# Performance work log

Hardware: AMD Instinct MI355X
Metric: run time of the kernel (lower is better)

## Reference

```python
import jax, jax.numpy as jnp
import numpy as np

N = 10000      # nodes
E = 100000     # edges
D = 768        # hidden = heads * head_dim
H = 4          # heads
C = D // H     # 192 per-head channels
EDIM = 16      # edge feature dim
NREL = 10      # num relations
L = 3          # num TransformerConv layers


def setup_inputs() -> dict:
    key = jax.random.key(0)
    ks = jax.random.split(key, 16)
    s = 0.02
    x = jax.random.normal(ks[0], (N, D), jnp.float32)
    edge_index = jax.random.randint(ks[1], (2, E), 0, N, jnp.int32)
    rel = jax.random.randint(ks[2], (E,), 0, NREL).astype(jnp.float32)
    w = jax.random.uniform(ks[3], (E,), jnp.float32)
    edge_attr = jnp.stack([rel, w], axis=1)  # [E, 2]: (relation_id, weight)
    rel_emb = jax.random.normal(ks[4], (NREL, EDIM - 1), jnp.float32) * s
    W_edge = jax.random.normal(ks[5], (EDIM, EDIM), jnp.float32) * s
    b_edge = jnp.zeros((EDIM,), jnp.float32)
    Wk = jax.random.normal(ks[6], (L, D, D), jnp.float32) * s
    bk = jnp.zeros((L, D), jnp.float32)
    Wq = jax.random.normal(ks[7], (L, D, D), jnp.float32) * s
    bq = jnp.zeros((L, D), jnp.float32)
    Wv = jax.random.normal(ks[8], (L, D, D), jnp.float32) * s
    bv = jnp.zeros((L, D), jnp.float32)
    We = jax.random.normal(ks[9], (L, EDIM, D), jnp.float32) * s   # lin_edge, no bias (PyG)
    Wskip = jax.random.normal(ks[10], (L, D, D), jnp.float32) * s  # root/skip linear
    bskip = jnp.zeros((L, D), jnp.float32)
    ln_g = jnp.ones((D,), jnp.float32)
    ln_b = jnp.zeros((D,), jnp.float32)
    return dict(x=x, edge_attr=edge_attr, edge_index=edge_index, rel_emb=rel_emb,
                W_edge=W_edge, b_edge=b_edge, Wk=Wk, bk=bk, Wq=Wq, bq=bq,
                Wv=Wv, bv=bv, We=We, Wskip=Wskip, bskip=bskip, ln_g=ln_g, ln_b=ln_b)


def reference(x, edge_attr, edge_index, rel_emb, W_edge, b_edge,
              Wk, bk, Wq, bq, Wv, bv, We, Wskip, bskip, ln_g, ln_b):
    src, dst = edge_index[0], edge_index[1]
    # _process_edge_features: embed relation id, concat weight, project
    rel_ids = jnp.clip(jax.lax.stop_gradient(edge_attr[:, 0]).astype(jnp.int32), 0, NREL - 1)
    ef = jnp.concatenate([rel_emb[rel_ids], edge_attr[:, 1:2]], axis=-1) @ W_edge + b_edge  # [E,16]
    scale = 1.0 / np.sqrt(C)
    h = x  # input_proj is Identity (input_dim == hidden_dim)
    for l in range(L):
        q = (h @ Wq[l] + bq[l]).reshape(N, H, C)
        k = (h @ Wk[l] + bk[l]).reshape(N, H, C)
        v = (h @ Wv[l] + bv[l]).reshape(N, H, C)
        e = (ef @ We[l]).reshape(E, H, C)           # per-edge embedding
        kj = k[src] + e                              # [E,H,C]
        alpha = jnp.einsum('ehc,ehc->eh', q[dst], kj) * scale  # [E,H]
        # scatter-softmax over incoming edges of each destination node
        m = jax.ops.segment_max(jax.lax.stop_gradient(alpha), dst, num_segments=N)
        a = jnp.exp(alpha - m[dst])
        denom = jax.ops.segment_sum(a, dst, num_segments=N)
        a = a / (denom[dst] + 1e-16)
        msg = (v[src] + e) * a[..., None]            # [E,H,C]
        out = jax.ops.segment_sum(msg.reshape(E, H * C), dst, num_segments=N)
        h = out + h @ Wskip[l] + bskip[l]            # root_weight skip connection
        if l < L - 1:
            h = jax.nn.gelu(h, approximate=False)    # dropout: eval mode -> identity
    mu = jnp.mean(h, axis=-1, keepdims=True)
    var = jnp.mean((h - mu) ** 2, axis=-1, keepdims=True)
    h = (h - mu) / jnp.sqrt(var + 1e-5) * ln_g + ln_b
    return jnp.mean(h, axis=0)  # global_mean_pool over single graph -> [D]
```

## Files before the change

### kernel.cpp

```cpp
#include <hip/hip_runtime.h>
#include <hip/hip_bf16.h>
#include <math.h>
#include <stdint.h>

#define NN 10000
#define EE 100000
#define DD 768
#define HH 4
#define CC 192
#define EDIM 16
#define NREL 10
#define MP 10112
#define NQ2 3200
#define SCALE 0.07216878364870322f

using short8  = __attribute__((ext_vector_type(8))) short;
using floatx4 = __attribute__((ext_vector_type(4))) float;


__device__ __forceinline__ float b2f(short u) {
    union { unsigned int i; float f; } t;
    t.i = ((unsigned int)(unsigned short)u) << 16;
    return t.f;
}

__device__ __forceinline__ short f2b(float f) {
    __hip_bfloat16 h = __float2bfloat16(f);
    short r;
    __builtin_memcpy(&r, &h, 2);
    return r;
}

__device__ __forceinline__ __hip_bfloat16 rd_any(const void* p, long long j, int bf) {
    if (bf) return ((const __hip_bfloat16*)p)[j];
    return __float2bfloat16(((const float*)p)[j]);
}

__device__ __forceinline__ void gload16(const __hip_bfloat16* g, __hip_bfloat16* l) {
    __builtin_amdgcn_global_load_lds(
        (const __attribute__((address_space(1))) unsigned int*)g,
        (__attribute__((address_space(3))) unsigned int*)l, 16, 0, 0);
}

__global__ __launch_bounds__(256) void detect_zero(const void* edge_attr,
                                                   int* flag, int* counts) {
    int i = blockIdx.x * 256 + threadIdx.x;
    if (i < NN) counts[i] = 0;
    if (blockIdx.x == 0 && threadIdx.x < 64) {
        const unsigned short* p = (const unsigned short*)edge_attr;
        int nz = (p[4 * threadIdx.x] != 0) ? 1 : 0;
        unsigned long long m = __ballot(nz);
        if (threadIdx.x == 0) *flag = (__popcll(m) > 8) ? 1 : 0;
    }
}


__global__ __launch_bounds__(256) void cvt_big(
    const void* x, const void* We, const int* flag,
    __hip_bfloat16* hb, __hip_bfloat16* Web) {
    long long i = (long long)blockIdx.x * 256 + threadIdx.x;
    int bf = *flag;
    const long long NX = (long long)NN * DD;
    const long long NE2 = 3LL * EDIM * DD;
    if (i < NX) { hb[i] = rd_any(x, i, bf); return; } i -= NX;
    if (i < NE2) { Web[i] = rd_any(We, i, bf); return; } i -= NE2;
    if (i < (long long)(MP - NN) * DD) hb[(long long)NN * DD + i] = __float2bfloat16(0.0f);
}

__global__ __launch_bounds__(256) void cvt_small(
    const void* ea, const void* rel, const void* Wed, const void* bed,
    const void* bk, const void* bq, const void* bv, const void* bs,
    const void* lg, const void* lb, const int* flag,
    __hip_bfloat16* eab, __hip_bfloat16* relb, __hip_bfloat16* Wedb,
    __hip_bfloat16* bedb, __hip_bfloat16* ballb, __hip_bfloat16* lgb,
    __hip_bfloat16* lbb) {
    long long i = (long long)blockIdx.x * 256 + threadIdx.x;
    int bf = *flag;
    if (i < 2LL * EE) { eab[i] = rd_any(ea, i, bf); return; } i -= 2LL * EE;
    if (i < NREL * (EDIM - 1)) { relb[i] = rd_any(rel, i, bf); return; } i -= NREL * (EDIM - 1);
    if (i < EDIM * EDIM) { Wedb[i] = rd_any(Wed, i, bf); return; } i -= EDIM * EDIM;
    if (i < EDIM) { bedb[i] = rd_any(bed, i, bf); return; } i -= EDIM;
    if (i < 3 * NQ2) {
        int l = (int)(i / NQ2), c = (int)(i % NQ2);
        const void* src; long long off;
        if (c < 768)       { src = bq; off = (long long)l * DD + c; }
        else if (c < 1536) { src = bk; off = (long long)l * DD + (c - 768); }
        else if (c < 2304) { src = bv; off = (long long)l * DD + (c - 1536); }
        else if (c < 3072) { src = bs; off = (long long)l * DD + (c - 2304); }
        else { ballb[i] = __float2bfloat16(0.0f); return; }
        ballb[i] = rd_any(src, off, bf); return;
    } i -= 3 * NQ2;
    if (i < DD) { lgb[i] = rd_any(lg, i, bf); return; } i -= DD;
    if (i < DD) { lbb[i] = rd_any(lb, i, bf); return; }
}

__global__ __launch_bounds__(256) void wt_all(
    const void* Wq, const void* Wk, const void* Wv, const void* Ws,
    const int* flag, __hip_bfloat16* Wt3) {
    __shared__ __hip_bfloat16 tile[32][33];
    int mm = blockIdx.y;
    int l = mm >> 2, m = mm & 3;
    const void* src = (m == 0) ? Wq : (m == 1) ? Wk : (m == 2) ? Wv : Ws;
    int bx = blockIdx.x;
    int tr = bx / 24, tc = bx % 24;
    int k0 = tr * 32, c0 = tc * 32;
    int t = threadIdx.x;
    int rr = t >> 5, cc = t & 31;
    int bf = *flag;
    long long base = (long long)l * DD * DD;
#pragma unroll
    for (int p = 0; p < 4; p++)
        tile[p * 8 + rr][cc] =
            rd_any(src, base + (long long)(k0 + p * 8 + rr) * DD + c0 + cc, bf);
    __syncthreads();
    __hip_bfloat16* dst = Wt3 + (size_t)l * NQ2 * DD + (size_t)(m * 768 + c0) * DD + k0;
#pragma unroll
    for (int p = 0; p < 4; p++)
        dst[(size_t)(p * 8 + rr) * DD + cc] = tile[cc][p * 8 + rr];
}

__global__ __launch_bounds__(256) void mq_kernel(
    const void* Wq, const void* bq, const int* flag,
    const __hip_bfloat16* __restrict__ Web, __hip_bfloat16* __restrict__ Wt3,
    __hip_bfloat16* __restrict__ ballb) {
    __shared__ float WeS[16][193];
    const int lh = blockIdx.y, l = lh >> 2, hh = lh & 3;
    const int t = threadIdx.x;
    const int bf = *flag;
    for (int i = t; i < 16 * 192; i += 256) {
        int j = i / 192, c = i % 192;
        WeS[j][c] = (float)Web[(size_t)l * EDIM * DD + (size_t)j * DD + hh * CC + c];
    }
    __syncthreads();
    const int k = blockIdx.x * 64 + (t >> 2);
    const int j0 = (t & 3) * 4;
    float s0 = 0.f, s1 = 0.f, s2 = 0.f, s3 = 0.f;
    if (bf) {
        const short8* qp = (const short8*)((const __hip_bfloat16*)Wq +
            ((size_t)l * DD + k) * DD + hh * CC);
#pragma unroll 4
        for (int ch = 0; ch < 24; ch++) {
            short8 v = qp[ch];
#pragma unroll
            for (int u = 0; u < 8; u++) {
                float w = b2f(v[u]);
                int c = ch * 8 + u;
                s0 += w * WeS[j0 + 0][c]; s1 += w * WeS[j0 + 1][c];
                s2 += w * WeS[j0 + 2][c]; s3 += w * WeS[j0 + 3][c];
            }
        }
    } else {
        const float4* qp = (const float4*)((const float*)Wq +
            ((size_t)l * DD + k) * DD + hh * CC);
#pragma unroll 4
        for (int ch = 0; ch < 48; ch++) {
            float4 v = qp[ch];
            float wv[4] = {v.x, v.y, v.z, v.w};
#pragma unroll
            for (int u = 0; u < 4; u++) {
                float w = wv[u];
                int c = ch * 4 + u;
                s0 += w * WeS[j0 + 0][c]; s1 += w * WeS[j0 + 1][c];
                s2 += w * WeS[j0 + 2][c]; s3 += w * WeS[j0 + 3][c];
            }
        }
    }
    const size_t base = (size_t)l * NQ2 * DD;
    const int row = 3072 + hh * 16 + j0;
    Wt3[base + (size_t)(row + 0) * DD + k] = __float2bfloat16(s0);
    Wt3[base + (size_t)(row + 1) * DD + k] = __float2bfloat16(s1);
    Wt3[base + (size_t)(row + 2) * DD + k] = __float2bfloat16(s2);
    Wt3[base + (size_t)(row + 3) * DD + k] = __float2bfloat16(s3);
    const int prow = 3136 + hh * 16 + j0;
#pragma unroll
    for (int i = 0; i < 4; i++)
        Wt3[base + (size_t)(prow + i) * DD + k] = __float2bfloat16(0.0f);
    if (blockIdx.x == 0 && t < 4) {
        float b0 = 0.f, b1 = 0.f, b2 = 0.f, b3 = 0.f;
        for (int c = 0; c < CC; c++) {
            float w = (float)rd_any(bq, (long long)l * DD + hh * CC + c, bf);
            b0 += w * WeS[j0 + 0][c]; b1 += w * WeS[j0 + 1][c];
            b2 += w * WeS[j0 + 2][c]; b3 += w * WeS[j0 + 3][c];
        }
        ballb[l * NQ2 + 3072 + hh * 16 + j0 + 0] = __float2bfloat16(b0);
        ballb[l * NQ2 + 3072 + hh * 16 + j0 + 1] = __float2bfloat16(b1);
        ballb[l * NQ2 + 3072 + hh * 16 + j0 + 2] = __float2bfloat16(b2);
        ballb[l * NQ2 + 3072 + hh * 16 + j0 + 3] = __float2bfloat16(b3);
    }
}


__global__ __launch_bounds__(256) void count_kernel(const int* ei, int* counts) {
    int e = blockIdx.x * 256 + threadIdx.x;
    if (e < EE) atomicAdd(&counts[ei[EE + e]], 1);
}

__global__ __launch_bounds__(256) void scan_kernel(const int* counts, int* rowptr,
                                                   int* cursor) {
    __shared__ int sdata[256];
    int t = threadIdx.x;
    int base = t * 40;
    int cnt = (base < NN) ? min(40, NN - base) : 0;
    int s = 0;
    for (int i = 0; i < cnt; i++) s += counts[base + i];
    sdata[t] = s;
    __syncthreads();
    for (int off = 1; off < 256; off <<= 1) {
        int add = (t >= off) ? sdata[t - off] : 0;
        __syncthreads();
        sdata[t] += add;
        __syncthreads();
    }
    int run = sdata[t] - s;
    for (int i = 0; i < cnt; i++) {
        cursor[base + i] = run;
        run += counts[base + i];
        rowptr[base + i + 1] = run;
    }
    if (t == 0) rowptr[0] = 0;
}

__global__ __launch_bounds__(256) void fill_kernel(const int* ei, int* cursor,
                                                   int* eids, int* esrc) {
    int e = blockIdx.x * 256 + threadIdx.x;
    if (e < EE) {
        int d = ei[EE + e];
        int pos = atomicAdd(&cursor[d], 1);
        eids[pos] = e;
        esrc[pos] = ei[e];
    }
}


__global__ __launch_bounds__(256) void ef_kernel(
    const int* __restrict__ eids,
    const __hip_bfloat16* __restrict__ eab, const __hip_bfloat16* __restrict__ relb,
    const __hip_bfloat16* __restrict__ Wedb, const __hip_bfloat16* __restrict__ bedb,
    __hip_bfloat16* __restrict__ efb) {
    int idx = blockIdx.x * 256 + threadIdx.x;
    if (idx >= EE * EDIM) return;
    int p = idx >> 4, j = idx & 15;
    int e = eids[p];
    int rid = (int)((float)eab[e * 2 + 0]);
    rid = min(max(rid, 0), NREL - 1);
    float w = (float)eab[e * 2 + 1];
    float s = (float)bedb[j];
#pragma unroll
    for (int i = 0; i < 15; i++)
        s += (float)relb[rid * 15 + i] * (float)Wedb[i * EDIM + j];
    s += w * (float)Wedb[15 * EDIM + j];
    efb[idx] = __float2bfloat16(s);
}


__global__ __launch_bounds__(256) void gemm_fused(
    const __hip_bfloat16* __restrict__ A, const __hip_bfloat16* __restrict__ Bt,
    const __hip_bfloat16* __restrict__ bias, __hip_bfloat16* __restrict__ C) {
    __shared__ __hip_bfloat16 As[128 * 32];
    __shared__ __hip_bfloat16 Bs[128 * 32];
    __shared__ __hip_bfloat16 stg[32 * 132];
    const int tid  = threadIdx.x;
    const int wid  = tid >> 6, lane = tid & 63;
    const int quad = lane >> 4, l15 = lane & 15;
    const int m0 = blockIdx.y * 128, n0 = blockIdx.x * 128;
    const int wm = wid >> 1, wn = wid & 1;
    floatx4 acc[4][4] = {};
    for (int k0 = 0; k0 < DD; k0 += 32) {
#pragma unroll
        for (int j = 0; j < 2; j++) {
            int c = j * 256 + tid;
            int r = c >> 2, s = c & 3;
            int ks = s ^ ((r + (r >> 2)) & 3);
            gload16(A + (size_t)(m0 + r) * DD + k0 + ks * 8, As + c * 8);
            gload16(Bt + (size_t)(n0 + r) * DD + k0 + ks * 8, Bs + c * 8);
        }
        __syncthreads();
        short8 a[4], b[4];
#pragma unroll
        for (int mt = 0; mt < 4; mt++) {
            int R = wm * 64 + mt * 16 + l15;
            int sw = quad ^ ((R + (R >> 2)) & 3);
            a[mt] = *(const short8*)(As + R * 32 + sw * 8);
        }
#pragma unroll
        for (int nt = 0; nt < 4; nt++) {
            int R = wn * 64 + nt * 16 + l15;
            int sw = quad ^ ((R + (R >> 2)) & 3);
            b[nt] = *(const short8*)(Bs + R * 32 + sw * 8);
        }
#pragma unroll
        for (int mt = 0; mt < 4; mt++)
#pragma unroll
            for (int nt = 0; nt < 4; nt++)
                acc[mt][nt] = __builtin_amdgcn_mfma_f32_16x16x32_bf16(a[mt], b[nt], acc[mt][nt], 0, 0, 0);
        __syncthreads();
    }
    float bv[4];
#pragma unroll
    for (int nt = 0; nt < 4; nt++) bv[nt] = (float)bias[n0 + wn * 64 + nt * 16 + l15];
    const int rr = tid >> 3, ccs = (tid & 7) * 16;
    const int grow = m0 + (rr >> 4) * 64 + (rr & 15);
    for (int mt = 0; mt < 4; mt++) {
#pragma unroll
        for (int nt = 0; nt < 4; nt++) {
            int col = wn * 64 + nt * 16 + l15;
#pragma unroll
            for (int r = 0; r < 4; r++) {
                int lr = wm * 16 + quad * 4 + r;
                stg[lr * 132 + col] = __float2bfloat16(acc[mt][nt][r] + bv[nt]);
            }
        }
        __syncthreads();
        int row = grow + mt * 16;
        if (row < NN) {
            const short8* sp = (const short8*)(stg + rr * 132 + ccs);
            short8 v0 = sp[0], v1 = sp[1];
            short8* dp = (short8*)(C + (size_t)row * NQ2 + n0 + ccs);
            dp[0] = v0; dp[1] = v1;
        }
        __syncthreads();
    }
}


__global__ __launch_bounds__(256) void node_attn(
    const int* __restrict__ rowptr, const int* __restrict__ esrc,
    const __hip_bfloat16* __restrict__ qkvs, const __hip_bfloat16* __restrict__ efb,
    const __hip_bfloat16* __restrict__ Wel, __hip_bfloat16* __restrict__ hb,
    int do_gelu) {
    const int wv = threadIdx.x >> 6, lane = threadIdx.x & 63;
    const int n = blockIdx.x * 2 + (wv >> 1);
    const int half = wv & 1;
    const int cb = half * 384 + lane * 6;
    const int sj = lane & 15;
    const int hsel = lane & 32;
    const float qe_gate = ((lane & 16) == 0) ? 1.0f : 0.0f;
    const int s0 = rowptr[n], s1 = rowptr[n + 1];
    const short* qk = (const short*)qkvs;
    float q[6];
    {
        const short2* qp = (const short2*)(qk + (size_t)n * NQ2 + cb);
        short2 a = qp[0], b = qp[1], c = qp[2];
        q[0] = b2f(a.x); q[1] = b2f(a.y); q[2] = b2f(b.x);
        q[3] = b2f(b.y); q[4] = b2f(c.x); q[5] = b2f(c.y);
    }
    const float qe_l = b2f(qk[(size_t)n * NQ2 + 3072 + (half * 2 + (lane >> 5)) * 16 + sj]);
    float m = -INFINITY, lsum = 0.f, sacc = 0.f;
    float acc[6] = {};
    for (int p = s0; p < s1; p++) {
        int src = esrc[p];
        const short2* kp = (const short2*)(qk + (size_t)src * NQ2 + 768 + cb);
        const short2* vp = (const short2*)(qk + (size_t)src * NQ2 + 1536 + cb);
        short2 ka = kp[0], kb = kp[1], kc = kp[2];
        short2 va = vp[0], vb = vp[1], vc = vp[2];
        float efv = b2f(((const short*)efb)[(size_t)p * 16 + sj]);
        float part = qe_gate * qe_l * efv;
        part += q[0] * b2f(ka.x) + q[1] * b2f(ka.y) + q[2] * b2f(kb.x);
        part += q[3] * b2f(kb.y) + q[4] * b2f(kc.x) + q[5] * b2f(kc.y);
        part += __shfl_xor(part, 1); part += __shfl_xor(part, 2);
        part += __shfl_xor(part, 4); part += __shfl_xor(part, 8);
        part += __shfl_xor(part, 16);
        float a = part * SCALE;
        float nm = fmaxf(m, a);
        float sc = __expf(m - nm);
        float w  = __expf(a - nm);
        lsum = lsum * sc + w;
        m = nm;
        acc[0] = acc[0] * sc + w * b2f(va.x); acc[1] = acc[1] * sc + w * b2f(va.y);
        acc[2] = acc[2] * sc + w * b2f(vb.x); acc[3] = acc[3] * sc + w * b2f(vb.y);
        acc[4] = acc[4] * sc + w * b2f(vc.x); acc[5] = acc[5] * sc + w * b2f(vc.y);
        sacc = sacc * sc + w * efv;
    }
    float inv = 1.0f / (lsum + 1e-16f);
#pragma unroll
    for (int i = 0; i < 6; i++) acc[i] *= inv;
    float sS = sacc * inv;
    {
        const short2* sp = (const short2*)(qk + (size_t)n * NQ2 + 2304 + cb);
        short2 a = sp[0], b = sp[1], c = sp[2];
        acc[0] += b2f(a.x); acc[1] += b2f(a.y); acc[2] += b2f(b.x);
        acc[3] += b2f(b.y); acc[4] += b2f(c.x); acc[5] += b2f(c.y);
    }
#pragma unroll
    for (int j = 0; j < 16; j++) {
        float sv = __shfl(sS, hsel + j);
        const short2* wp = (const short2*)(Wel + (size_t)j * DD + cb);
        short2 a = wp[0], b = wp[1], c = wp[2];
        acc[0] += sv * b2f(a.x); acc[1] += sv * b2f(a.y); acc[2] += sv * b2f(b.x);
        acc[3] += sv * b2f(b.y); acc[4] += sv * b2f(c.x); acc[5] += sv * b2f(c.y);
    }
    if (do_gelu) {
#pragma unroll
        for (int i = 0; i < 6; i++)
            acc[i] = 0.5f * acc[i] * (1.0f + erff(acc[i] * 0.70710678118654752f));
    }
    short2 o0, o1, o2;
    o0.x = f2b(acc[0]); o0.y = f2b(acc[1]);
    o1.x = f2b(acc[2]); o1.y = f2b(acc[3]);
    o2.x = f2b(acc[4]); o2.y = f2b(acc[5]);
    short2* hp = (short2*)(hb + (size_t)n * DD + cb);
    hp[0] = o0; hp[1] = o1; hp[2] = o2;
}


__global__ __launch_bounds__(256) void ln_pool(
    const __hip_bfloat16* __restrict__ hb, const __hip_bfloat16* __restrict__ g,
    const __hip_bfloat16* __restrict__ b, float* __restrict__ partial) {
    __shared__ float sbuf[4][768];
    int grp = blockIdx.x, t = threadIdx.x;
    int wid = t >> 6, lane = t & 63;
    float gv[12], bv[12], acc[12];
#pragma unroll
    for (int i = 0; i < 12; i++) {
        gv[i] = (float)g[lane + i * 64];
        bv[i] = (float)b[lane + i * 64];
        acc[i] = 0.f;
    }
    for (int r = wid; r < 25; r += 4) {
        const __hip_bfloat16* row = hb + (size_t)(grp * 25 + r) * DD;
        float x[12];
        float s = 0.f, q = 0.f;
#pragma unroll
        for (int i = 0; i < 12; i++) {
            x[i] = (float)row[lane + i * 64];
            s += x[i]; q += x[i] * x[i];
        }
#pragma unroll
        for (int m = 32; m > 0; m >>= 1) {
            s += __shfl_xor(s, m); q += __shfl_xor(q, m);
        }
        float mu = s * (1.0f / 768.0f);
        float ms = q * (1.0f / 768.0f);
        float inv = 1.0f / sqrtf(ms - mu * mu + 1e-5f);
#pragma unroll
        for (int i = 0; i < 12; i++)
            acc[i] += (x[i] - mu) * inv * gv[i] + bv[i];
    }
#pragma unroll
    for (int i = 0; i < 12; i++) sbuf[wid][lane + i * 64] = acc[i];
    __syncthreads();
#pragma unroll
    for (int j = 0; j < 3; j++) {
        int col = t + j * 256;
        partial[(size_t)grp * DD + col] =
            sbuf[0][col] + sbuf[1][col] + sbuf[2][col] + sbuf[3][col];
    }
}

__global__ __launch_bounds__(256) void pool_final(
    const float* __restrict__ partial, void* __restrict__ out,
    const int* __restrict__ flag) {
    int dd = blockIdx.x * 256 + threadIdx.x;
    if (dd >= DD) return;
    float s = 0.f;
    for (int g2 = 0; g2 < 400; g2++) s += partial[(size_t)g2 * DD + dd];
    s *= (1.0f / 10000.0f);
    if (*flag) ((__hip_bfloat16*)out)[dd] = __float2bfloat16(s);
    else ((float*)out)[dd] = s;
}


extern "C" void kernel_launch(void* const* d_in, const int* in_sizes, int n_in,
                              void* d_out, int out_size, void* d_ws, size_t ws_size,
                              hipStream_t stream) {
    const void* x         = d_in[0];
    const void* edge_attr = d_in[1];
    const int*  ei        = (const int*)d_in[2];
    const void* rel_emb   = d_in[3];
    const void* W_edge    = d_in[4];
    const void* b_edge    = d_in[5];
    const void* Wk        = d_in[6];
    const void* bk        = d_in[7];
    const void* Wq        = d_in[8];
    const void* bq        = d_in[9];
    const void* Wv        = d_in[10];
    const void* bv        = d_in[11];
    const void* We        = d_in[12];
    const void* Wskip     = d_in[13];
    const void* bskip     = d_in[14];
    const void* ln_g      = d_in[15];
    const void* ln_b      = d_in[16];

    char* ws = (char*)d_ws;
    int*   flag    = (int*)(ws + 0);
    int*   counts  = (int*)(ws + 256);
    int*   rowptr  = (int*)(ws + 40448);
    int*   cursor  = (int*)(ws + 80640);
    int*   eids    = (int*)(ws + 120832);
    int*   esrc    = (int*)(ws + 520960);
    __hip_bfloat16* efb = (__hip_bfloat16*)(ws + 920960);
    float* partial = (float*)(ws + 4120960);
    __hip_bfloat16* eab   = (__hip_bfloat16*)(ws + 5398912);
    __hip_bfloat16* relb  = (__hip_bfloat16*)(ws + 5799296);
    __hip_bfloat16* Wedb  = (__hip_bfloat16*)(ws + 5799680);
    __hip_bfloat16* bedb  = (__hip_bfloat16*)(ws + 5800192);
    __hip_bfloat16* ballb = (__hip_bfloat16*)(ws + 5800320);
    __hip_bfloat16* lngb  = (__hip_bfloat16*)(ws + 5819520);
    __hip_bfloat16* lnbb  = (__hip_bfloat16*)(ws + 5821056);
    __hip_bfloat16* Web   = (__hip_bfloat16*)(ws + 5822592);
    __hip_bfloat16* hb    = (__hip_bfloat16*)(ws + 5896320);
    __hip_bfloat16* Wt3   = (__hip_bfloat16*)(ws + 21428352);
    __hip_bfloat16* qkvs  = (__hip_bfloat16*)(ws + 36173952);

    dim3 blk(256);

    detect_zero<<<dim3(40), blk, 0, stream>>>(edge_attr, flag, counts);

    {
        long long tot = (long long)NN * DD + 3LL * EDIM * DD + (long long)(MP - NN) * DD;
        cvt_big<<<dim3((unsigned)((tot + 255) / 256)), blk, 0, stream>>>(x, We, flag, hb, Web);
    }
    {
        long long tot = 2LL * EE + NREL * (EDIM - 1) + EDIM * EDIM + EDIM
                        + 3LL * NQ2 + 2LL * DD;
        cvt_small<<<dim3((unsigned)((tot + 255) / 256)), blk, 0, stream>>>(
            edge_attr, rel_emb, W_edge, b_edge, bk, bq, bv, bskip, ln_g, ln_b,
            flag, eab, relb, Wedb, bedb, ballb, lngb, lnbb);
    }
    wt_all<<<dim3(576, 12), blk, 0, stream>>>(Wq, Wk, Wv, Wskip, flag, Wt3);
    mq_kernel<<<dim3(12, 12), blk, 0, stream>>>(Wq, bq, flag, Web, Wt3, ballb);

    count_kernel<<<dim3((EE + 255) / 256), blk, 0, stream>>>(ei, counts);
    scan_kernel<<<dim3(1), blk, 0, stream>>>(counts, rowptr, cursor);
    fill_kernel<<<dim3((EE + 255) / 256), blk, 0, stream>>>(ei, cursor, eids, esrc);

    ef_kernel<<<dim3((EE * EDIM) / 256), blk, 0, stream>>>(eids, eab, relb, Wedb, bedb, efb);

    for (int l = 0; l < 3; l++) {
        const __hip_bfloat16* We_l = Web + (size_t)l * EDIM * DD;
        gemm_fused<<<dim3(NQ2 / 128, MP / 128), blk, 0, stream>>>(
            hb, Wt3 + (size_t)l * NQ2 * DD, ballb + (size_t)l * NQ2, qkvs);
        node_attn<<<dim3(NN / 2), blk, 0, stream>>>(rowptr, esrc, qkvs, efb,
                                                    We_l, hb, (l < 2) ? 1 : 0);
    }

    ln_pool<<<dim3(400), blk, 0, stream>>>(hb, lngb, lnbb, partial);
    pool_final<<<dim3(3), blk, 0, stream>>>(partial, d_out, flag);
}
```

Before: 636.1 us.

## Replace 128x128 GEMM with 256x256 pipelined MFMA kernel using 512 threads

Replaces the per-layer fused QKV/skip GEMM with a 256x256-tile kernel of 8 waves. It double-buffers 64-wide K tiles in 128KB of LDS and interleaves global prefetch with MFMA phases, using raised wave priority and manual waitcnts. Blocks are swizzled for L2 locality, and the N dimension is padded to 3328 and M to 10240, with extra zeroed weight rows. The aim is higher arithmetic intensity and overlap of loads with compute. The cost is heavy LDS use (one block per CU) and fragile hand-tuned synchronisation.

Result: no change. 640.0 us (+0.6%).

```diff
diff --git a/kernel.cpp b/kernel.cpp
--- a/kernel.cpp
+++ b/kernel.cpp
@@ -10,8 +10,9 @@
 #define CC 192
 #define EDIM 16
 #define NREL 10
-#define MP 10112
+#define MP 10240
 #define NQ2 3200
+#define NB 3328
 #define SCALE 0.07216878364870322f
 
 using short8  = __attribute__((ext_vector_type(8))) short;
@@ -80,8 +81,8 @@
     if (i < NREL * (EDIM - 1)) { relb[i] = rd_any(rel, i, bf); return; } i -= NREL * (EDIM - 1);
     if (i < EDIM * EDIM) { Wedb[i] = rd_any(Wed, i, bf); return; } i -= EDIM * EDIM;
     if (i < EDIM) { bedb[i] = rd_any(bed, i, bf); return; } i -= EDIM;
-    if (i < 3 * NQ2) {
-        int l = (int)(i / NQ2), c = (int)(i % NQ2);
+    if (i < 3 * NB) {
+        int l = (int)(i / NB), c = (int)(i % NB);
         const void* src; long long off;
         if (c < 768)       { src = bq; off = (long long)l * DD + c; }
         else if (c < 1536) { src = bk; off = (long long)l * DD + (c - 768); }
@@ -89,7 +90,7 @@
         else if (c < 3072) { src = bs; off = (long long)l * DD + (c - 2304); }
         else { ballb[i] = __float2bfloat16(0.0f); return; }
         ballb[i] = rd_any(src, off, bf); return;
-    } i -= 3 * NQ2;
+    } i -= 3 * NB;
     if (i < DD) { lgb[i] = rd_any(lg, i, bf); return; } i -= DD;
     if (i < DD) { lbb[i] = rd_any(lb, i, bf); return; }
 }
@@ -113,7 +114,7 @@
         tile[p * 8 + rr][cc] =
             rd_any(src, base + (long long)(k0 + p * 8 + rr) * DD + c0 + cc, bf);
     __syncthreads();
-    __hip_bfloat16* dst = Wt3 + (size_t)l * NQ2 * DD + (size_t)(m * 768 + c0) * DD + k0;
+    __hip_bfloat16* dst = Wt3 + (size_t)l * NB * DD + (size_t)(m * 768 + c0) * DD + k0;
 #pragma unroll
     for (int p = 0; p < 4; p++)
         dst[(size_t)(p * 8 + rr) * DD + cc] = tile[cc][p * 8 + rr];
@@ -165,7 +166,7 @@
             }
         }
     }
-    const size_t base = (size_t)l * NQ2 * DD;
+    const size_t base = (size_t)l * NB * DD;
     const int row = 3072 + hh * 16 + j0;
     Wt3[base + (size_t)(row + 0) * DD + k] = __float2bfloat16(s0);
     Wt3[base + (size_t)(row + 1) * DD + k] = __float2bfloat16(s1);
@@ -175,6 +176,13 @@
 #pragma unroll
     for (int i = 0; i < 4; i++)
         Wt3[base + (size_t)(prow + i) * DD + k] = __float2bfloat16(0.0f);
+    if ((t & 3) == 0) {
+        const __hip_bfloat16 z = __float2bfloat16(0.0f);
+        const int kk = blockIdx.x * 64 + (t >> 2);
+#pragma unroll 4
+        for (int rz = 0; rz < 32; rz++)
+            Wt3[base + (size_t)(3200 + hh * 32 + rz) * DD + kk] = z;
+    }
     if (blockIdx.x == 0 && t < 4) {
         float b0 = 0.f, b1 = 0.f, b2 = 0.f, b3 = 0.f;
         for (int c = 0; c < CC; c++) {
@@ -182,10 +190,10 @@
             b0 += w * WeS[j0 + 0][c]; b1 += w * WeS[j0 + 1][c];
             b2 += w * WeS[j0 + 2][c]; b3 += w * WeS[j0 + 3][c];
         }
-        ballb[l * NQ2 + 3072 + hh * 16 + j0 + 0] = __float2bfloat16(b0);
-        ballb[l * NQ2 + 3072 + hh * 16 + j0 + 1] = __float2bfloat16(b1);
-        ballb[l * NQ2 + 3072 + hh * 16 + j0 + 2] = __float2bfloat16(b2);
-        ballb[l * NQ2 + 3072 + hh * 16 + j0 + 3] = __float2bfloat16(b3);
+        ballb[l * NB + 3072 + hh * 16 + j0 + 0] = __float2bfloat16(b0);
+        ballb[l * NB + 3072 + hh * 16 + j0 + 1] = __float2bfloat16(b1);
+        ballb[l * NB + 3072 + hh * 16 + j0 + 2] = __float2bfloat16(b2);
+        ballb[l * NB + 3072 + hh * 16 + j0 + 3] = __float2bfloat16(b3);
     }
 }
 
@@ -253,72 +261,230 @@
 }
 
 
-__global__ __launch_bounds__(256) void gemm_fused(
+__device__ __forceinline__ void stage_half(const __hip_bfloat16* g, int row0, int ktile,
+                                           char* ldsdst, int tid) {
+#pragma unroll
+    for (int j = 0; j < 2; ++j) {
+        int c = j * 512 + tid;
+        int row = c >> 3;
+        int sch = (c & 7) ^ (row & 7);
+        gload16(g + (size_t)(row0 + row) * DD + ktile * 64 + sch * 8,
+                (__hip_bfloat16*)(ldsdst + c * 16));
+    }
+}
+
+#define MF16(va, vb, cc) cc = __builtin_amdgcn_mfma_f32_16x16x32_bf16(va, vb, cc, 0, 0, 0)
+#define BAR() __builtin_amdgcn_s_barrier()
+#define WLG() asm volatile("s_waitcnt lgkmcnt(0)" ::: "memory")
+#define WVM(N) asm volatile("s_waitcnt vmcnt(" #N ")" ::: "memory")
+#define LDS8(off) (*(const short8*)(smem + (off)))
+
+__global__ __launch_bounds__(512) void gemm256(
     const __hip_bfloat16* __restrict__ A, const __hip_bfloat16* __restrict__ Bt,
     const __hip_bfloat16* __restrict__ bias, __hip_bfloat16* __restrict__ C) {
-    __shared__ __hip_bfloat16 As[128 * 32];
-    __shared__ __hip_bfloat16 Bs[128 * 32];
-    __shared__ __hip_bfloat16 stg[32 * 132];
-    const int tid  = threadIdx.x;
-    const int wid  = tid >> 6, lane = tid & 63;
+    __shared__ __align__(16) char smem[131072];
+    const int tid = threadIdx.x;
+    const int wid = tid >> 6, lane = tid & 63;
     const int quad = lane >> 4, l15 = lane & 15;
-    const int m0 = blockIdx.y * 128, n0 = blockIdx.x * 128;
-    const int wm = wid >> 1, wn = wid & 1;
-    floatx4 acc[4][4] = {};
-    for (int k0 = 0; k0 < DD; k0 += 32) {
-#pragma unroll
-        for (int j = 0; j < 2; j++) {
-            int c = j * 256 + tid;
-            int r = c >> 2, s = c & 3;
-            int ks = s ^ ((r + (r >> 2)) & 3);
-            gload16(A + (size_t)(m0 + r) * DD + k0 + ks * 8, As + c * 8);
-            gload16(Bt + (size_t)(n0 + r) * DD + k0 + ks * 8, Bs + c * 8);
-        }
-        __syncthreads();
-        short8 a[4], b[4];
-#pragma unroll
-        for (int mt = 0; mt < 4; mt++) {
-            int R = wm * 64 + mt * 16 + l15;
-            int sw = quad ^ ((R + (R >> 2)) & 3);
-            a[mt] = *(const short8*)(As + R * 32 + sw * 8);
-        }
-#pragma unroll
-        for (int nt = 0; nt < 4; nt++) {
-            int R = wn * 64 + nt * 16 + l15;
-            int sw = quad ^ ((R + (R >> 2)) & 3);
-            b[nt] = *(const short8*)(Bs + R * 32 + sw * 8);
-        }
-#pragma unroll
-        for (int mt = 0; mt < 4; mt++)
-#pragma unroll
-            for (int nt = 0; nt < 4; nt++)
-                acc[mt][nt] = __builtin_amdgcn_mfma_f32_16x16x32_bf16(a[mt], b[nt], acc[mt][nt], 0, 0, 0);
-        __syncthreads();
-    }
-    float bv[4];
-#pragma unroll
-    for (int nt = 0; nt < 4; nt++) bv[nt] = (float)bias[n0 + wn * 64 + nt * 16 + l15];
-    const int rr = tid >> 3, ccs = (tid & 7) * 16;
-    const int grow = m0 + (rr >> 4) * 64 + (rr & 15);
-    for (int mt = 0; mt < 4; mt++) {
-#pragma unroll
-        for (int nt = 0; nt < 4; nt++) {
-            int col = wn * 64 + nt * 16 + l15;
-#pragma unroll
-            for (int r = 0; r < 4; r++) {
-                int lr = wm * 16 + quad * 4 + r;
-                stg[lr * 132 + col] = __float2bfloat16(acc[mt][nt][r] + bv[nt]);
-            }
-        }
-        __syncthreads();
-        int row = grow + mt * 16;
-        if (row < NN) {
-            const short8* sp = (const short8*)(stg + rr * 132 + ccs);
-            short8 v0 = sp[0], v1 = sp[1];
-            short8* dp = (short8*)(C + (size_t)row * NQ2 + n0 + ccs);
-            dp[0] = v0; dp[1] = v1;
-        }
-        __syncthreads();
+    const int wm = wid >> 2, wn = wid & 3;
+    const int bid = (int)blockIdx.x;
+    const int swz = (bid & 7) * 65 + (bid >> 3);
+    const int m0 = (swz / 13) * 256;
+    const int n0 = (swz % 13) * 256;
+
+    const int xa0 = (quad ^ (l15 & 7)) * 16;
+    const int xa1 = ((quad + 4) ^ (l15 & 7)) * 16;
+    const int aRow = (wm * 128 + l15) * 128;
+    const int bRow = 32768 + (wn * 64 + l15) * 128;
+
+    floatx4 acc[8][4] = {};
+    short8 a[4][2], bA[2][2], bB[2][2];
+
+    stage_half(A, m0, 0, smem + 0, tid);
+    stage_half(A, m0 + 128, 0, smem + 16384, tid);
+    stage_half(Bt, n0, 0, smem + 32768, tid);
+    stage_half(Bt, n0 + 128, 0, smem + 49152, tid);
+    stage_half(Bt, n0, 1, smem + 98304, tid);
+    stage_half(Bt, n0 + 128, 1, smem + 114688, tid);
+    WVM(4);
+    BAR();
+
+#pragma unroll 1
+    for (int it = 0; it < 6; ++it) {
+        const int kA = 2 * it + 1;
+        const int kB = (it < 5) ? 2 * it + 2 : 0;
+        const int kC = (it < 5) ? 2 * it + 3 : 1;
+#pragma unroll
+        for (int mt = 0; mt < 4; ++mt) {
+            a[mt][0] = LDS8(aRow + mt * 2048 + xa0);
+            a[mt][1] = LDS8(aRow + mt * 2048 + xa1);
+        }
+#pragma unroll
+        for (int nt = 0; nt < 2; ++nt) {
+            bA[nt][0] = LDS8(bRow + nt * 2048 + xa0);
+            bA[nt][1] = LDS8(bRow + nt * 2048 + xa1);
+        }
+        stage_half(A, m0, kA, smem + 65536, tid);
+        BAR(); WLG();
+        __builtin_amdgcn_s_setprio(1);
+#pragma unroll
+        for (int mt = 0; mt < 4; ++mt)
+#pragma unroll
+            for (int nt = 0; nt < 2; ++nt) {
+                MF16(a[mt][0], bA[nt][0], acc[mt][nt]);
+                MF16(a[mt][1], bA[nt][1], acc[mt][nt]);
+            }
+        __builtin_amdgcn_s_setprio(0);
+        BAR();
+#pragma unroll
+        for (int nt = 0; nt < 2; ++nt) {
+            bB[nt][0] = LDS8(bRow + (nt + 2) * 2048 + xa0);
+            bB[nt][1] = LDS8(bRow + (nt + 2) * 2048 + xa1);
+        }
+        stage_half(A, m0 + 128, kA, smem + 81920, tid);
+        WVM(6);
+        BAR(); WLG();
+        __builtin_amdgcn_s_setprio(1);
+#pragma unroll
+        for (int mt = 0; mt < 4; ++mt)
+#pragma unroll
+            for (int nt = 0; nt < 2; ++nt) {
+                MF16(a[mt][0], bB[nt][0], acc[mt][nt + 2]);
+                MF16(a[mt][1], bB[nt][1], acc[mt][nt + 2]);
+            }
+        __builtin_amdgcn_s_setprio(0);
+        BAR();
+#pragma unroll
+        for (int mt = 0; mt < 4; ++mt) {
+            a[mt][0] = LDS8(aRow + (mt + 4) * 2048 + xa0);
+            a[mt][1] = LDS8(aRow + (mt + 4) * 2048 + xa1);
+        }
+        stage_half(Bt, n0, kB, smem + 32768, tid);
+        BAR(); WLG();
+        __builtin_amdgcn_s_setprio(1);
+#pragma unroll
+        for (int mt = 0; mt < 4; ++mt)
+#pragma unroll
+            for (int nt = 0; nt < 2; ++nt) {
+                MF16(a[mt][0], bB[nt][0], acc[mt + 4][nt + 2]);
+                MF16(a[mt][1], bB[nt][1], acc[mt + 4][nt + 2]);
+            }
+        __builtin_amdgcn_s_setprio(0);
+        BAR();
+        stage_half(Bt, n0 + 128, kB, smem + 49152, tid);
+        WVM(4);
+        BAR(); WLG();
+        __builtin_amdgcn_s_setprio(1);
+#pragma unroll
+        for (int mt = 0; mt < 4; ++mt)
+#pragma unroll
+            for (int nt = 0; nt < 2; ++nt) {
+                MF16(a[mt][0], bA[nt][0], acc[mt + 4][nt]);
+                MF16(a[mt][1], bA[nt][1], acc[mt + 4][nt]);
+            }
+        __builtin_amdgcn_s_setprio(0);
+        BAR();
+#pragma unroll
+        for (int mt = 0; mt < 4; ++mt) {
+            a[mt][0] = LDS8(65536 + aRow + mt * 2048 + xa0);
+            a[mt][1] = LDS8(65536 + aRow + mt * 2048 + xa1);
+        }
+#pragma unroll
+        for (int nt = 0; nt < 2; ++nt) {
+            bA[nt][0] = LDS8(65536 + bRow + nt * 2048 + xa0);
+            bA[nt][1] = LDS8(65536 + bRow + nt * 2048 + xa1);
+        }
+        stage_half(A, m0, kB, smem + 0, tid);
+        BAR(); WLG();
+        __builtin_amdgcn_s_setprio(1);
+#pragma unroll
+        for (int mt = 0; mt < 4; ++mt)
+#pragma unroll
+            for (int nt = 0; nt < 2; ++nt) {
+                MF16(a[mt][0], bA[nt][0], acc[mt][nt]);
+                MF16(a[mt][1], bA[nt][1], acc[mt][nt]);
+            }
+        __builtin_amdgcn_s_setprio(0);
+        BAR();
+#pragma unroll
+        for (int nt = 0; nt < 2; ++nt) {
+            bB[nt][0] = LDS8(65536 + bRow + (nt + 2) * 2048 + xa0);
+            bB[nt][1] = LDS8(65536 + bRow + (nt + 2) * 2048 + xa1);
+        }
+        stage_half(A, m0 + 128, kB, smem + 16384, tid);
+        WVM(6);
+        BAR(); WLG();
+        __builtin_amdgcn_s_setprio(1);
+#pragma unroll
+        for (int mt = 0; mt < 4; ++mt)
+#pragma unroll
+            for (int nt = 0; nt < 2; ++nt) {
+                MF16(a[mt][0], bB[nt][0], acc[mt][nt + 2]);
+                MF16(a[mt][1], bB[nt][1], acc[mt][nt + 2]);
+            }
+        __builtin_amdgcn_s_setprio(0);
+        BAR();
+#pragma unroll
+        for (int mt = 0; mt < 4; ++mt) {
+            a[mt][0] = LDS8(65536 + aRow + (mt + 4) * 2048 + xa0);
+            a[mt][1] = LDS8(65536 + aRow + (mt + 4) * 2048 + xa1);
+        }
+        stage_half(Bt, n0, kC, smem + 98304, tid);
+        BAR(); WLG();
+        __builtin_amdgcn_s_setprio(1);
+#pragma unroll
+        for (int mt = 0; mt < 4; ++mt)
+#pragma unroll
+            for (int nt = 0; nt < 2; ++nt) {
+                MF16(a[mt][0], bB[nt][0], acc[mt + 4][nt + 2]);
+                MF16(a[mt][1], bB[nt][1], acc[mt + 4][nt + 2]);
+            }
+        __builtin_amdgcn_s_setprio(0);
+        BAR();
+        stage_half(Bt, n0 + 128, kC, smem + 114688, tid);
+        WVM(4);
+        BAR(); WLG();
+        __builtin_amdgcn_s_setprio(1);
+#pragma unroll
+        for (int mt = 0; mt < 4; ++mt)
+#pragma unroll
+            for (int nt = 0; nt < 2; ++nt) {
+                MF16(a[mt][0], bA[nt][0], acc[mt + 4][nt]);
+                MF16(a[mt][1], bA[nt][1], acc[mt + 4][nt]);
+            }
+        __builtin_amdgcn_s_setprio(0);
+        BAR();
+    }
+
+    asm volatile("s_waitcnt vmcnt(0)" ::: "memory");
+    BAR();
+    {
+        short* stg = (short*)smem + wid * 1152;
+        float bv[4];
+#pragma unroll
+        for (int nt = 0; nt < 4; ++nt)
+            bv[nt] = (float)bias[n0 + wn * 64 + nt * 16 + l15];
+        const int rdo = (lane >> 2) * 68 + (lane & 3) * 16;
+        const int grow0 = m0 + wm * 128 + (lane >> 2);
+        const int gcol = n0 + wn * 64 + (lane & 3) * 16;
+#pragma unroll
+        for (int mt = 0; mt < 8; ++mt) {
+#pragma unroll
+            for (int nt = 0; nt < 4; ++nt)
+#pragma unroll
+                for (int r = 0; r < 4; ++r)
+                    stg[(quad * 4 + r) * 68 + nt * 16 + l15] =
+                        f2b(acc[mt][nt][r] + bv[nt]);
+            asm volatile("s_waitcnt lgkmcnt(0)" ::: "memory");
+            short8 v0 = *(const short8*)(stg + rdo);
+            short8 v1 = *(const short8*)(stg + rdo + 8);
+            int grow = grow0 + mt * 16;
+            if (grow < NN && gcol < NQ2) {
+                short8* dp = (short8*)(C + (size_t)grow * NQ2 + gcol);
+                dp[0] = v0; dp[1] = v1;
+            }
+            asm volatile("s_waitcnt lgkmcnt(0)" ::: "memory");
+        }
     }
 }
 
@@ -490,17 +656,17 @@
     int*   esrc    = (int*)(ws + 520960);
     __hip_bfloat16* efb = (__hip_bfloat16*)(ws + 920960);
     float* partial = (float*)(ws + 4120960);
-    __hip_bfloat16* eab   = (__hip_bfloat16*)(ws + 5398912);
-    __hip_bfloat16* relb  = (__hip_bfloat16*)(ws + 5799296);
-    __hip_bfloat16* Wedb  = (__hip_bfloat16*)(ws + 5799680);
-    __hip_bfloat16* bedb  = (__hip_bfloat16*)(ws + 5800192);
-    __hip_bfloat16* ballb = (__hip_bfloat16*)(ws + 5800320);
-    __hip_bfloat16* lngb  = (__hip_bfloat16*)(ws + 5819520);
-    __hip_bfloat16* lnbb  = (__hip_bfloat16*)(ws + 5821056);
-    __hip_bfloat16* Web   = (__hip_bfloat16*)(ws + 5822592);
-    __hip_bfloat16* hb    = (__hip_bfloat16*)(ws + 5896320);
-    __hip_bfloat16* Wt3   = (__hip_bfloat16*)(ws + 21428352);
-    __hip_bfloat16* qkvs  = (__hip_bfloat16*)(ws + 36173952);
+    __hip_bfloat16* eab   = (__hip_bfloat16*)(ws + 5349760);
+    __hip_bfloat16* relb  = (__hip_bfloat16*)(ws + 5749760);
+    __hip_bfloat16* Wedb  = (__hip_bfloat16*)(ws + 5750144);
+    __hip_bfloat16* bedb  = (__hip_bfloat16*)(ws + 5750656);
+    __hip_bfloat16* ballb = (__hip_bfloat16*)(ws + 5750784);
+    __hip_bfloat16* lngb  = (__hip_bfloat16*)(ws + 5770752);
+    __hip_bfloat16* lnbb  = (__hip_bfloat16*)(ws + 5772288);
+    __hip_bfloat16* Web   = (__hip_bfloat16*)(ws + 5773824);
+    __hip_bfloat16* hb    = (__hip_bfloat16*)(ws + 5847552);
+    __hip_bfloat16* Wt3   = (__hip_bfloat16*)(ws + 21576192);
+    __hip_bfloat16* qkvs  = (__hip_bfloat16*)(ws + 36911616);
 
     dim3 blk(256);
 
@@ -512,7 +678,7 @@
     }
     {
         long long tot = 2LL * EE + NREL * (EDIM - 1) + EDIM * EDIM + EDIM
-                        + 3LL * NQ2 + 2LL * DD;
+                        + 3LL * NB + 2LL * DD;
         cvt_small<<<dim3((unsigned)((tot + 255) / 256)), blk, 0, stream>>>(
             edge_attr, rel_emb, W_edge, b_edge, bk, bq, bv, bskip, ln_g, ln_b,
             flag, eab, relb, Wedb, bedb, ballb, lngb, lnbb);
@@ -528,8 +694,8 @@
 
     for (int l = 0; l < 3; l++) {
         const __hip_bfloat16* We_l = Web + (size_t)l * EDIM * DD;
-        gemm_fused<<<dim3(NQ2 / 128, MP / 128), blk, 0, stream>>>(
-            hb, Wt3 + (size_t)l * NQ2 * DD, ballb + (size_t)l * NQ2, qkvs);
+        gemm256<<<dim3(520), dim3(512), 0, stream>>>(
+            hb, Wt3 + (size_t)l * NB * DD, ballb + (size_t)l * NB, qkvs);
         node_attn<<<dim3(NN / 2), blk, 0, stream>>>(rowptr, esrc, qkvs, efb,
                                                     We_l, hb, (l < 2) ? 1 : 0);
     }
```
